# Kernel tuning notes

Hardware: AMD Instinct MI355X
Metric: run time of the kernel (lower is better)

The kernel has to match this reference:

```python
import jax, jax.numpy as jnp
import numpy as np

EPS = 1e-5


def _bn_silu(x, gamma, beta):
    # train-mode BatchNorm2d (biased batch stats over N,H,W) followed by SiLU
    m = jnp.mean(x, axis=(0, 2, 3), keepdims=True)
    v = jnp.var(x, axis=(0, 2, 3), keepdims=True)
    y = gamma[None, :, None, None] * (x - m) * jax.lax.rsqrt(v + EPS) + beta[None, :, None, None]
    return y * jax.nn.sigmoid(y)


def _deform_conv2d(x, offset, w, b):
    # x: [B,C,H,W]; offset: [B,2*9,H,W] as (dy,dx) pairs per 3x3 tap; w: [Co,C,3,3]
    B, C, H, W = x.shape
    Co = w.shape[0]
    off = offset.reshape(B, 9, 2, H, W)
    k = jnp.arange(9)
    ky = (k // 3 - 1).astype(x.dtype)  # kernel tap offsets, pad=1 so centered
    kx = (k % 3 - 1).astype(x.dtype)
    py = jnp.arange(H, dtype=x.dtype)[None, None, :, None] + ky[None, :, None, None] + off[:, :, 0]
    px = jnp.arange(W, dtype=x.dtype)[None, None, None, :] + kx[None, :, None, None] + off[:, :, 1]
    y0 = jnp.floor(py)
    x0 = jnp.floor(px)
    wy1 = py - y0
    wx1 = px - x0
    xf = x.reshape(B, C, H * W)

    def corner(yi, xi, cw):
        # zero-padded bilinear corner: mask out-of-bounds taps via weight
        valid = (yi >= 0) & (yi < H) & (xi >= 0) & (xi < W)
        idx = jnp.clip(yi, 0, H - 1) * W + jnp.clip(xi, 0, W - 1)
        g = jnp.take_along_axis(xf, idx.reshape(B, 1, -1), axis=2).reshape(B, C, 9, H, W)
        return g * (cw * valid.astype(x.dtype))[:, None]

    y0i = y0.astype(jnp.int32)
    x0i = x0.astype(jnp.int32)
    s = corner(y0i, x0i, (1 - wy1) * (1 - wx1))
    s = s + corner(y0i, x0i + 1, (1 - wy1) * wx1)
    s = s + corner(y0i + 1, x0i, wy1 * (1 - wx1))
    s = s + corner(y0i + 1, x0i + 1, wy1 * wx1)
    out = jnp.einsum('bckhw,ock->bohw', s, w.reshape(Co, C, 9))
    return out + b[None, :, None, None]


def _conv_transpose(x, w, stride, pad):
    # torch ConvTranspose2d: weight layout [Cin, Cout, kh, kw]
    k = w.shape[2]
    wf = jnp.flip(w, (2, 3)).transpose(1, 0, 2, 3)  # -> OIHW, spatially flipped
    p = k - 1 - pad
    return jax.lax.conv_general_dilated(
        x, wf, (1, 1), [(p, p), (p, p)], lhs_dilation=(stride, stride),
        dimension_numbers=('NCHW', 'OIHW', 'NCHW'))


def setup_inputs() -> dict:
    key = jax.random.key(0)
    ks = jax.random.split(key, 4)
    B, C, Co, H, W = 16, 256, 256, 32, 32
    r = lambda k, s, sc: jax.random.normal(k, s, jnp.float32) * sc
    return {
        'x': r(ks[0], (B, C, H, W), 1.0),
        'w_off': r(ks[1], (18, C, 3, 3), 0.01),
        'b_off': jnp.zeros((18,), jnp.float32),
        'w_def': r(ks[2], (Co, C, 3, 3), 0.02),
        'b_def': jnp.zeros((Co,), jnp.float32),
        'gamma1': jnp.ones((Co,), jnp.float32),
        'beta1': jnp.zeros((Co,), jnp.float32),
        'w_dc': r(ks[3], (Co, Co, 4, 4), 0.02),
        'gamma2': jnp.ones((Co,), jnp.float32),
        'beta2': jnp.zeros((Co,), jnp.float32),
    }


def reference(x, w_off, b_off, w_def, b_def, gamma1, beta1, w_dc, gamma2, beta2):
    offset = jax.lax.conv_general_dilated(
        x, w_off, (1, 1), [(1, 1), (1, 1)],
        dimension_numbers=('NCHW', 'OIHW', 'NCHW')) + b_off[None, :, None, None]
    y = _deform_conv2d(x, offset, w_def, b_def)
    y = _bn_silu(y, gamma1, beta1)
    y = _conv_transpose(y, w_dc, 2, 1)
    return _bn_silu(y, gamma2, beta2)
```

## Files before the change

### kernel.cpp

```cpp
#include <hip/hip_runtime.h>
#include <math.h>

#ifdef __has_builtin
#if __has_builtin(__builtin_amdgcn_global_load_lds)
#define HAS_GLL 1
#endif
#endif
#ifndef HAS_GLL
#define HAS_GLL 0
#endif

typedef __attribute__((ext_vector_type(8))) short short8v;
typedef __attribute__((ext_vector_type(4))) float float4v;

__device__ __forceinline__ unsigned short f2bf(float f) {
    unsigned int u = __float_as_uint(f);
    u += 0x7fffu + ((u >> 16) & 1u);
    return (unsigned short)(u >> 16);
}

__device__ __forceinline__ float silu(float y) { return y / (1.f + expf(-y)); }

__device__ __forceinline__ void stage1k(const void* gsrc, void* ldsbase) {
#if HAS_GLL
    __builtin_amdgcn_global_load_lds((const __attribute__((address_space(1))) unsigned int*)gsrc,
                                     (__attribute__((address_space(3))) unsigned int*)ldsbase,
                                     16, 0, 0);
#else
    int lane = threadIdx.x & 63;
    *(float4*)((char*)ldsbase + lane * 16) = *(const float4*)gsrc;
#endif
}

__global__ __launch_bounds__(256) void k_prep_all(const float* __restrict__ w_def,
                                                  const float* __restrict__ w_dc,
                                                  const float* __restrict__ w_off,
                                                  const float* __restrict__ x,
                                                  unsigned short* __restrict__ A1,
                                                  unsigned short* __restrict__ A2,
                                                  unsigned short* __restrict__ A2off,
                                                  unsigned short* __restrict__ xT) {
    int blk = blockIdx.x;
    int t = threadIdx.x;
    __shared__ unsigned short tl[32][36];
    if (blk < 4096) {
        int i = blk * 256 + t;
        int ci = i & 255;
        int tq = (i >> 8) & 3;
        int co = (i >> 10) & 255;
        int p  = i >> 18;
        int ph = p >> 1, pw = p & 1;
        int ty = tq >> 1, tx = tq & 1;
        int kh = 2 * ty + 1 - ph;
        int kw = 2 * tx + 1 - pw;
        A2[i] = f2bf(w_dc[((ci * 256 + co) * 4 + kh) * 4 + kw]);
    } else if (blk < 6400) {
        int i = (blk - 4096) * 256 + t;
        A1[i] = f2bf(w_def[i]);
    } else if (blk < 6688) {
        int i = (blk - 6400) * 256 + t;
        int slot = i & 31;
        int oc = (i >> 5) & 31;
        int rest = i >> 10;
        int tap = rest % 9;
        int cc8 = rest / 9;
        int cgrp = (slot >> 3) ^ ((oc >> 1) & 3);
        int c = cc8 * 32 + (cgrp << 3) + (slot & 7);
        unsigned short v = 0;
        if (oc < 18) v = f2bf(w_off[(size_t)oc * 2304 + c * 9 + tap]);
        A2off[i] = v;
    } else {
        int blk2 = blk - 6688;
        int hw0 = (blk2 & 31) * 32;
        int c0 = ((blk2 >> 5) & 7) * 32;
        int b = blk2 >> 8;
        {
            int c_l = t >> 3, w4 = (t & 7) * 4;
            float4 v = *(const float4*)&x[(size_t)((b * 256 + c0 + c_l) * 1024) + hw0 + w4];
            tl[c_l][w4 + 0] = f2bf(v.x);
            tl[c_l][w4 + 1] = f2bf(v.y);
            tl[c_l][w4 + 2] = f2bf(v.z);
            tl[c_l][w4 + 3] = f2bf(v.w);
        }
        __syncthreads();
        {
            int hw_l = t >> 3, c4 = (t & 7) * 4;
            unsigned int s0 = tl[c4 + 0][hw_l];
            unsigned int s1 = tl[c4 + 1][hw_l];
            unsigned int s2 = tl[c4 + 2][hw_l];
            unsigned int s3 = tl[c4 + 3][hw_l];
            uint2 pk;
            pk.x = s0 | (s1 << 16);
            pk.y = s2 | (s3 << 16);
            *(uint2*)&xT[(size_t)((b * 1024 + hw0 + hw_l) * 256) + c0 + c4] = pk;
        }
    }
}

__global__ __launch_bounds__(256) void k_off_gemm(const unsigned short* __restrict__ A2off,
                                                  const unsigned short* __restrict__ xT,
                                                  const float* __restrict__ b_off,
                                                  float* __restrict__ off) {
    int hp = blockIdx.x, b = blockIdx.y;
    int h0 = hp * 2;
    int t = threadIdx.x;
    int lane = t & 63, wid = t >> 6;
    int l15 = lane & 15, g = lane >> 4;
    int swg = (l15 >> 1) & 3;
    __shared__ __align__(16) unsigned short As[9 * 32 * 32];
    __shared__ __align__(16) unsigned short Bsx[4 * 34 * 32];
    float4v acc[2];
    float4v z = {0.f, 0.f, 0.f, 0.f};
    acc[0] = z; acc[1] = z;

    int pos = wid * 16 + l15;
    int py = pos >> 5, px = pos & 31;

    for (int cc8 = 0; cc8 < 8; ++cc8) {
        __syncthreads();
        for (int idx = t; idx < 1152; idx += 256)
            stage1k(A2off + (size_t)cc8 * 9216 + idx * 8, (char*)As + idx * 16);
        for (int idx = t; idx < 544; idx += 256) {
            int r = idx / 136;
            int rem = idx - r * 136;
            int col = rem >> 2;
            int sgrp = rem & 3;
            int grp = sgrp ^ ((col >> 1) & 3);
            int h = h0 - 1 + r;
            int w = col - 1;
            uint4 v = {0u, 0u, 0u, 0u};
            if (h >= 0 && h < 32 && w >= 0 && w < 32)
                v = *(const uint4*)&xT[(size_t)((b * 1024 + h * 32 + w) * 256) + cc8 * 32 + grp * 8];
            *(uint4*)((char*)Bsx + ((r * 34 + col) << 6) + (sgrp << 4)) = v;
        }
        __syncthreads();
#pragma unroll
        for (int tap = 0; tap < 9; ++tap) {
            int ky = tap / 3, kx = tap - ky * 3;
            int col = px + kx;
            int rowr = py + ky;
            short8v bbf = *(const short8v*)((const char*)Bsx + ((rowr * 34 + col) << 6) +
                                            ((g ^ ((col >> 1) & 3)) << 4));
            short8v a0 = *(const short8v*)((const char*)As + tap * 2048 + l15 * 64 + ((g ^ swg) << 4));
            short8v a1 = *(const short8v*)((const char*)As + tap * 2048 + (16 + l15) * 64 + ((g ^ swg) << 4));
            acc[0] = __builtin_amdgcn_mfma_f32_16x16x32_bf16(a0, bbf, acc[0], 0, 0, 0);
            acc[1] = __builtin_amdgcn_mfma_f32_16x16x32_bf16(a1, bbf, acc[1], 0, 0, 0);
        }
    }
    int h = h0 + py;
#pragma unroll
    for (int r = 0; r < 4; ++r) {
        int oc = g * 4 + r;
        off[((size_t)(b * 18 + oc) << 10) + (h << 5) + px] = acc[0][r] + b_off[oc];
    }
    if (g == 0) {
#pragma unroll
        for (int r = 0; r < 2; ++r) {
            int oc = 16 + r;
            off[((size_t)(b * 18 + oc) << 10) + (h << 5) + px] = acc[1][r] + b_off[oc];
        }
    }
}

__global__ __launch_bounds__(576) void k_sample(const float* __restrict__ x,
                                                const float* __restrict__ off,
                                                unsigned short* __restrict__ S) {
    int cg = blockIdx.x, b = blockIdx.y, half = blockIdx.z;
    int cbase = cg * 8;
    int t = threadIdx.x;
    int k = t >> 6, lane = t & 63;
    __shared__ __align__(16) unsigned int xpl[4 * 1156];
    __shared__ __align__(16) unsigned short sS[72 * 66];

    for (int u = t; u < 1024; u += 576) {
        int p = u >> 8, row = (u >> 3) & 31, cq = (u & 7) << 2;
        const float* src0 = x + ((size_t)(b * 256 + cbase + 2 * p) << 10) + (row << 5) + cq;
        float4 a = *(const float4*)src0;
        float4 c = *(const float4*)(src0 + 1024);
        uint4 pk;
        pk.x = (unsigned int)f2bf(a.x) | ((unsigned int)f2bf(c.x) << 16);
        pk.y = (unsigned int)f2bf(a.y) | ((unsigned int)f2bf(c.y) << 16);
        pk.z = (unsigned int)f2bf(a.z) | ((unsigned int)f2bf(c.z) << 16);
        pk.w = (unsigned int)f2bf(a.w) | ((unsigned int)f2bf(c.w) << 16);
        *(uint4*)&xpl[p * 1156 + row * 36 + cq] = pk;
    }

    int wr_row = t / 9, wr_q = t - wr_row * 9;
    const float* offk0 = off + ((size_t)(b * 18 + 2 * k) << 10);
    const float* offk1 = off + ((size_t)(b * 18 + 2 * k + 1) << 10);
    int ky = k / 3 - 1, kx = k % 3 - 1;
    __syncthreads();

    for (int ci = 0; ci < 8; ++ci) {
        int chunk = half * 8 + ci;
        int pos = chunk * 64 + lane;
        int h = pos >> 5, w = pos & 31;
        float dy = offk0[pos];
        float dx = offk1[pos];
        float py = (float)(h + ky) + dy;
        float px = (float)(w + kx) + dx;
        float fy = floorf(py), fx = floorf(px);
        int y0i = (int)fy, x0i = (int)fx;
        float wy = py - fy, wxf = px - fx;
        float vy0 = (y0i >= 0 && y0i < 32) ? 1.f : 0.f;
        float vy1 = (y0i >= -1 && y0i < 31) ? 1.f : 0.f;
        float vx0 = (x0i >= 0 && x0i < 32) ? 1.f : 0.f;
        float vx1 = (x0i >= -1 && x0i < 31) ? 1.f : 0.f;
        int y0c = min(max(y0i, 0), 31), y1c = min(max(y0i + 1, 0), 31);
        int x0c = min(max(x0i, 0), 31), x1c = min(max(x0i + 1, 0), 31);
        float w00 = (1.f - wy) * (1.f - wxf) * vy0 * vx0;
        float w01 = (1.f - wy) * wxf * vy0 * vx1;
        float w10 = wy * (1.f - wxf) * vy1 * vx0;
        float w11 = wy * wxf * vy1 * vx1;
        int a00 = y0c * 36 + x0c, a01 = y0c * 36 + x1c;
        int a10 = y1c * 36 + x0c, a11 = y1c * 36 + x1c;
#pragma unroll
        for (int p = 0; p < 4; ++p) {
            const unsigned int* pl = xpl + p * 1156;
            unsigned int c00 = pl[a00], c01 = pl[a01], c10 = pl[a10], c11 = pl[a11];
            float e00 = __uint_as_float(c00 << 16), o00 = __uint_as_float(c00 & 0xFFFF0000u);
            float e01 = __uint_as_float(c01 << 16), o01 = __uint_as_float(c01 & 0xFFFF0000u);
            float e10 = __uint_as_float(c10 << 16), o10 = __uint_as_float(c10 & 0xFFFF0000u);
            float e11 = __uint_as_float(c11 << 16), o11 = __uint_as_float(c11 & 0xFFFF0000u);
            float ve = w00 * e00 + w01 * e01 + w10 * e10 + w11 * e11;
            float vo = w00 * o00 + w01 * o01 + w10 * o10 + w11 * o11;
            sS[((2 * p) * 9 + k) * 66 + lane] = f2bf(ve);
            sS[((2 * p + 1) * 9 + k) * 66 + lane] = f2bf(vo);
        }
        __syncthreads();
        {
            int basekc = wr_q * 8;
            unsigned int s0 = sS[(basekc + 0) * 66 + wr_row];
            unsigned int s1 = sS[(basekc + 1) * 66 + wr_row];
            unsigned int s2 = sS[(basekc + 2) * 66 + wr_row];
            unsigned int s3 = sS[(basekc + 3) * 66 + wr_row];
            unsigned int s4 = sS[(basekc + 4) * 66 + wr_row];
            unsigned int s5 = sS[(basekc + 5) * 66 + wr_row];
            unsigned int s6 = sS[(basekc + 6) * 66 + wr_row];
            unsigned int s7 = sS[(basekc + 7) * 66 + wr_row];
            uint4 qv;
            qv.x = s0 | (s1 << 16);
            qv.y = s2 | (s3 << 16);
            qv.z = s4 | (s5 << 16);
            qv.w = s6 | (s7 << 16);
            *(uint4*)(S + (size_t)(b * 1024 + chunk * 64 + wr_row) * 2304 + cg * 72 + wr_q * 8) = qv;
        }
        __syncthreads();
    }
}

__global__ __launch_bounds__(256) void k_gemm1(const unsigned short* __restrict__ A1,
                                               const unsigned short* __restrict__ S,
                                               const float* __restrict__ b_def,
                                               float* __restrict__ y1,
                                               float* __restrict__ pstats1) {
    int nb = blockIdx.x, mb = blockIdx.y;
    int t = threadIdx.x;
    int lane = t & 63, wid = t >> 6;
    int wm = wid >> 1, wn = wid & 1;
    int l15 = lane & 15, g = lane >> 4;
    __shared__ __align__(16) unsigned short As[2][8192];
    __shared__ __align__(16) unsigned short Bs[2][4096];
    int m0 = mb * 128, n0 = nb * 64;
    int b = n0 >> 10, pos0 = n0 & 1023;

    const unsigned short* srcA[4];
    int dA[4];
    const unsigned short* srcB[2];
    int dB[2];
#pragma unroll
    for (int it = 0; it < 4; ++it) {
        int idx = t + it * 256;
        int r = idx >> 3, s8 = idx & 7, c = s8 ^ (r & 7);
        srcA[it] = A1 + (size_t)(m0 + r) * 2304 + c * 8;
        dA[it] = idx * 8;
    }
#pragma unroll
    for (int it = 0; it < 2; ++it) {
        int idx = t + it * 256;
        int r = idx >> 3, s8 = idx & 7, c = s8 ^ (r & 7);
        srcB[it] = S + (size_t)(n0 + r) * 2304 + c * 8;
        dB[it] = idx * 8;
    }

    float4v acc[4][2];
    float4v z = {0.f, 0.f, 0.f, 0.f};
#pragma unroll
    for (int i = 0; i < 4; ++i) { acc[i][0] = z; acc[i][1] = z; }

#pragma unroll
    for (int it = 0; it < 4; ++it) stage1k(srcA[it], &As[0][dA[it]]);
#pragma unroll
    for (int it = 0; it < 2; ++it) stage1k(srcB[it], &Bs[0][dB[it]]);
    __syncthreads();

    for (int step = 0; step < 36; ++step) {
        int cur = step & 1;
        if (step < 35) {
            int koff = (step + 1) * 64;
#pragma unroll
            for (int it = 0; it < 4; ++it) stage1k(srcA[it] + koff, &As[cur ^ 1][dA[it]]);
#pragma unroll
            for (int it = 0; it < 2; ++it) stage1k(srcB[it] + koff, &Bs[cur ^ 1][dB[it]]);
        }
        __builtin_amdgcn_s_setprio(1);
#pragma unroll
        for (int kk = 0; kk < 2; ++kk) {
            short8v a[4], bb[2];
#pragma unroll
            for (int mi = 0; mi < 4; ++mi) {
                int row = wm * 64 + mi * 16 + l15;
                int slot = ((kk << 2) + g) ^ (row & 7);
                a[mi] = *(const short8v*)((const char*)&As[cur][0] + row * 128 + slot * 16);
            }
#pragma unroll
            for (int ni = 0; ni < 2; ++ni) {
                int row = wn * 32 + ni * 16 + l15;
                int slot = ((kk << 2) + g) ^ (row & 7);
                bb[ni] = *(const short8v*)((const char*)&Bs[cur][0] + row * 128 + slot * 16);
            }
#pragma unroll
            for (int mi = 0; mi < 4; ++mi)
#pragma unroll
                for (int ni = 0; ni < 2; ++ni)
                    acc[mi][ni] = __builtin_amdgcn_mfma_f32_16x16x32_bf16(a[mi], bb[ni], acc[mi][ni], 0, 0, 0);
        }
        __builtin_amdgcn_s_setprio(0);
        __syncthreads();
    }

    float* sred  = (float*)&As[0][0];
    float* s2red = sred + 256;
#pragma unroll
    for (int mi = 0; mi < 4; ++mi) {
#pragma unroll
        for (int r = 0; r < 4; ++r) {
            int co = m0 + wm * 64 + mi * 16 + g * 4 + r;
            float bv = b_def[co];
            float* dst = y1 + ((size_t)(b * 256 + co) << 10) + pos0;
            float s = 0.f, s2 = 0.f;
#pragma unroll
            for (int ni = 0; ni < 2; ++ni) {
                float v = acc[mi][ni][r] + bv;
                dst[wn * 32 + ni * 16 + l15] = v;
                s += v;
                s2 += v * v;
            }
#pragma unroll
            for (int m = 8; m >= 1; m >>= 1) {
                s  += __shfl_xor(s, m, 64);
                s2 += __shfl_xor(s2, m, 64);
            }
            if (l15 == 0) {
                int col = wm * 64 + mi * 16 + g * 4 + r;
                sred[col * 2 + wn]  = s;
                s2red[col * 2 + wn] = s2;
            }
        }
    }
    __syncthreads();
    if (t < 128) {
        float s  = sred[t * 2] + sred[t * 2 + 1];
        float s2 = s2red[t * 2] + s2red[t * 2 + 1];
        int ch = m0 + t;
        pstats1[ch * 256 + nb] = s;
        pstats1[65536 + ch * 256 + nb] = s2;
    }
}

__global__ __launch_bounds__(256) void k_gemm2(const unsigned short* __restrict__ A2,
                                               const unsigned short* __restrict__ y1T,
                                               unsigned short* __restrict__ outP,
                                               float* __restrict__ pstats2) {
    int nb = blockIdx.x, mb = blockIdx.y, p = blockIdx.z;
    int ph = p >> 1, pw = p & 1;
    int t = threadIdx.x;
    int lane = t & 63, wid = t >> 6;
    int wm = wid >> 1, wn = wid & 1;
    int l15 = lane & 15, g = lane >> 4;
    __shared__ __align__(16) unsigned short As[2][8192];
    __shared__ __align__(16) unsigned short Bs[2][8192];
    int m0 = mb * 128, n0 = nb * 128;
    int b = n0 >> 10, pos0 = n0 & 1023, oh0 = pos0 >> 5;

    int dtab[4];
#pragma unroll
    for (int tap = 0; tap < 4; ++tap) {
        int ty = tap >> 1, tx = tap & 1;
        int dy = ph ? (1 - ty) : (-ty);
        int dx = pw ? (1 - tx) : (-tx);
        dtab[tap] = (dy * 34 + dx) * 256;
    }
    const unsigned short* srcA[4];
    const unsigned short* srcB[4];
    int dstoff[4];
#pragma unroll
    for (int it = 0; it < 4; ++it) {
        int idx = t + it * 256;
        int r = idx >> 3, s8 = idx & 7, c = s8 ^ (r & 7);
        srcA[it] = A2 + (size_t)(p * 256 + m0 + r) * 1024 + c * 8;
        int ih = oh0 + (r >> 5) + 1;
        int iw = (r & 31) + 1;
        srcB[it] = y1T + ((size_t)(b * 34 + ih) * 34 + iw) * 256 + c * 8;
        dstoff[it] = idx * 8;
    }

    float4v acc[4][4];
    float4v z = {0.f, 0.f, 0.f, 0.f};
#pragma unroll
    for (int i = 0; i < 4; ++i)
#pragma unroll
        for (int j = 0; j < 4; ++j) acc[i][j] = z;

#pragma unroll
    for (int it = 0; it < 4; ++it) {
        stage1k(srcA[it], &As[0][dstoff[it]]);
        stage1k(srcB[it] + dtab[0], &Bs[0][dstoff[it]]);
    }
    __syncthreads();

#pragma unroll
    for (int step = 0; step < 16; ++step) {
        int cur = step & 1;
        if (step < 15) {
            int ns = step + 1;
            int tap = ns >> 2;
            int koff = ns * 64;
            int boff = dtab[tap] + (ns & 3) * 64;
#pragma unroll
            for (int it = 0; it < 4; ++it) {
                stage1k(srcA[it] + koff, &As[cur ^ 1][dstoff[it]]);
                stage1k(srcB[it] + boff, &Bs[cur ^ 1][dstoff[it]]);
            }
        }
        __builtin_amdgcn_s_setprio(1);
#pragma unroll
        for (int kk = 0; kk < 2; ++kk) {
            short8v a[4], bb[4];
#pragma unroll
            for (int mi = 0; mi < 4; ++mi) {
                int row = wm * 64 + mi * 16 + l15;
                int slot = ((kk << 2) + g) ^ (row & 7);
                a[mi] = *(const short8v*)((const char*)&As[cur][0] + row * 128 + slot * 16);
            }
#pragma unroll
            for (int ni = 0; ni < 4; ++ni) {
                int row = wn * 64 + ni * 16 + l15;
                int slot = ((kk << 2) + g) ^ (row & 7);
                bb[ni] = *(const short8v*)((const char*)&Bs[cur][0] + row * 128 + slot * 16);
            }
#pragma unroll
            for (int mi = 0; mi < 4; ++mi)
#pragma unroll
                for (int ni = 0; ni < 4; ++ni)
                    acc[mi][ni] = __builtin_amdgcn_mfma_f32_16x16x32_bf16(a[mi], bb[ni], acc[mi][ni], 0, 0, 0);
        }
        __builtin_amdgcn_s_setprio(0);
        __syncthreads();
    }
#pragma unroll
    for (int mi = 0; mi < 4; ++mi) {
#pragma unroll
        for (int r = 0; r < 4; ++r) {
            int co = m0 + wm * 64 + mi * 16 + g * 4 + r;
            unsigned short* dst = outP + ((size_t)((p * 16 + b) * 256 + co) << 10) + pos0;
#pragma unroll
            for (int ni = 0; ni < 4; ++ni)
                dst[wn * 64 + ni * 16 + l15] = f2bf(acc[mi][ni][r]);
        }
    }
    float* sred  = (float*)&As[0][0];
    float* s2red = sred + 256;
#pragma unroll
    for (int mi = 0; mi < 4; ++mi) {
#pragma unroll
        for (int r = 0; r < 4; ++r) {
            float s = 0.f, s2 = 0.f;
#pragma unroll
            for (int ni = 0; ni < 4; ++ni) {
                float v = acc[mi][ni][r];
                s += v;
                s2 += v * v;
            }
#pragma unroll
            for (int m = 8; m >= 1; m >>= 1) {
                s  += __shfl_xor(s, m, 64);
                s2 += __shfl_xor(s2, m, 64);
            }
            if (l15 == 0) {
                int col = wm * 64 + mi * 16 + g * 4 + r;
                sred[col * 2 + wn]  = s;
                s2red[col * 2 + wn] = s2;
            }
        }
    }
    __syncthreads();
    if (t < 128) {
        float s  = sred[t * 2] + sred[t * 2 + 1];
        float s2 = s2red[t * 2] + s2red[t * 2 + 1];
        int row = p * 128 + nb;
        int ch = m0 + t;
        pstats2[ch * 512 + row] = s;
        pstats2[131072 + ch * 512 + row] = s2;
    }
}

__global__ __launch_bounds__(256) void k_bnfin_par(const float* __restrict__ pstats, int nparts,
                                                   float n,
                                                   float* __restrict__ mean, float* __restrict__ rstd) {
    int ch = blockIdx.x;
    int t = threadIdx.x;
    float s = 0.f, s2 = 0.f;
    for (int j = t; j < nparts; j += 256) {
        s  += pstats[ch * nparts + j];
        s2 += pstats[256 * nparts + ch * nparts + j];
    }
    __shared__ float rs[256], rs2[256];
    rs[t] = s; rs2[t] = s2;
    __syncthreads();
    for (int d = 128; d > 0; d >>= 1) {
        if (t < d) { rs[t] += rs[t + d]; rs2[t] += rs2[t + d]; }
        __syncthreads();
    }
    if (t == 0) {
        float m = rs[0] / n;
        float var = rs2[0] / n - m * m;
        mean[ch] = m;
        rstd[ch] = rsqrtf(var + 1e-5f);
    }
}

__global__ __launch_bounds__(256) void k_bnsilu_padT(const float* __restrict__ y1,
                                                     const float* __restrict__ mean,
                                                     const float* __restrict__ rstd,
                                                     const float* __restrict__ gamma,
                                                     const float* __restrict__ beta,
                                                     unsigned short* __restrict__ y1T) {
    int py = blockIdx.x, cg = blockIdx.y, b = blockIdx.z;
    int c0 = cg * 32;
    int t = threadIdx.x;
    uint2 zz; zz.x = 0u; zz.y = 0u;
    if (py == 0 || py == 33) {
        for (int u = t; u < 272; u += 256) {
            int col = u >> 3, c4 = (u & 7) * 4;
            *(uint2*)&y1T[((size_t)(b * 34 + py) * 34 + col) * 256 + c0 + c4] = zz;
        }
        return;
    }
    __shared__ unsigned short tl[32][36];
    int iy = py - 1;
    {
        int c_l = t >> 3, px4 = (t & 7) * 4;
        int ch = c0 + c_l;
        float m = mean[ch], rs = rstd[ch], ga = gamma[ch], be = beta[ch];
        float4 v = *(const float4*)&y1[(size_t)((b * 256 + ch) << 10) + (iy << 5) + px4];
        tl[c_l][px4 + 0] = f2bf(silu(ga * (v.x - m) * rs + be));
        tl[c_l][px4 + 1] = f2bf(silu(ga * (v.y - m) * rs + be));
        tl[c_l][px4 + 2] = f2bf(silu(ga * (v.z - m) * rs + be));
        tl[c_l][px4 + 3] = f2bf(silu(ga * (v.w - m) * rs + be));
    }
    __syncthreads();
    {
        int px = t >> 3, c4 = (t & 7) * 4;
        unsigned int s0 = tl[c4 + 0][px];
        unsigned int s1 = tl[c4 + 1][px];
        unsigned int s2 = tl[c4 + 2][px];
        unsigned int s3 = tl[c4 + 3][px];
        uint2 pk;
        pk.x = s0 | (s1 << 16);
        pk.y = s2 | (s3 << 16);
        *(uint2*)&y1T[((size_t)(b * 34 + py) * 34 + (px + 1)) * 256 + c0 + c4] = pk;
    }
    if (t < 16) {
        int col = (t >> 3) ? 33 : 0;
        int c4 = (t & 7) * 4;
        *(uint2*)&y1T[((size_t)(b * 34 + py) * 34 + col) * 256 + c0 + c4] = zz;
    }
}

__global__ __launch_bounds__(256) void k_bnsilu_out(const unsigned short* __restrict__ outP,
                                                    const float* __restrict__ mean,
                                                    const float* __restrict__ rstd,
                                                    const float* __restrict__ gamma,
                                                    const float* __restrict__ beta,
                                                    float* __restrict__ out) {
    unsigned int i = blockIdx.x * 256 + threadIdx.x;
    int ow4 = i & 15;
    int oh = (i >> 4) & 63;
    int co = (i >> 10) & 255;
    int b  = i >> 18;
    int p0 = (oh & 1) * 2;
    int pos = ((oh >> 1) << 5) + ow4 * 2;
    const unsigned short* pl0 = outP + ((size_t)((p0 * 16 + b) * 256 + co) << 10) + pos;
    const unsigned short* pl1 = pl0 + ((size_t)16 * 256 << 10);
    unsigned int ue = *(const unsigned int*)pl0;
    unsigned int uo = *(const unsigned int*)pl1;
    float ex = __uint_as_float(ue << 16), ey = __uint_as_float(ue & 0xFFFF0000u);
    float ox = __uint_as_float(uo << 16), oy = __uint_as_float(uo & 0xFFFF0000u);
    float m = mean[co], rs = rstd[co], ga = gamma[co], be = beta[co];
    float4 v;
    v.x = silu(ga * (ex - m) * rs + be);
    v.y = silu(ga * (ox - m) * rs + be);
    v.z = silu(ga * (ey - m) * rs + be);
    v.w = silu(ga * (oy - m) * rs + be);
    *(float4*)&out[((size_t)(b * 256 + co) << 12) + (oh << 6) + ow4 * 4] = v;
}

extern "C" void kernel_launch(void* const* d_in, const int* in_sizes, int n_in,
                              void* d_out, int out_size, void* d_ws, size_t ws_size,
                              hipStream_t stream) {
    const float* x      = (const float*)d_in[0];
    const float* w_off  = (const float*)d_in[1];
    const float* b_off  = (const float*)d_in[2];
    const float* w_def  = (const float*)d_in[3];
    const float* b_def  = (const float*)d_in[4];
    const float* gamma1 = (const float*)d_in[5];
    const float* beta1  = (const float*)d_in[6];
    const float* w_dc   = (const float*)d_in[7];
    const float* gamma2 = (const float*)d_in[8];
    const float* beta2  = (const float*)d_in[9];
    float* out = (float*)d_out;

    char* base = (char*)d_ws;
    unsigned short* S    = (unsigned short*)base;
    float*          y1   = (float*)(base + 75497472);
    unsigned short* y1T  = (unsigned short*)(base + 92274688);
    unsigned short* A1   = (unsigned short*)(base + 101744640);
    unsigned short* A2   = (unsigned short*)(base + 102924288);
    float*          off  = (float*)(base + 105021440);
    float*          stats = (float*)(base + 106201088);
    float* mean1 = stats, *rstd1 = stats + 256, *mean2 = stats + 512, *rstd2 = stats + 768;
    float* pstats1 = off;
    float* pstats2 = off;
    unsigned short* xT    = (unsigned short*)base;
    unsigned short* A2off = (unsigned short*)(base + 8388608);
    unsigned short* outP = (unsigned short*)base;

    k_prep_all<<<10784, 256, 0, stream>>>(w_def, w_dc, w_off, x, A1, A2, A2off, xT);
    k_off_gemm<<<dim3(16, 16), 256, 0, stream>>>(A2off, xT, b_off, off);
    k_sample<<<dim3(32, 16, 2), 576, 0, stream>>>(x, off, S);
    k_gemm1<<<dim3(256, 2), 256, 0, stream>>>(A1, S, b_def, y1, pstats1);
    k_bnfin_par<<<256, 256, 0, stream>>>(pstats1, 256, 16384.f, mean1, rstd1);
    k_bnsilu_padT<<<dim3(34, 8, 16), 256, 0, stream>>>(y1, mean1, rstd1, gamma1, beta1, y1T);
    k_gemm2<<<dim3(128, 2, 4), 256, 0, stream>>>(A2, y1T, outP, pstats2);
    k_bnfin_par<<<256, 256, 0, stream>>>(pstats2, 512, 65536.f, mean2, rstd2);
    k_bnsilu_out<<<16384, 256, 0, stream>>>(outP, mean2, rstd2, gamma2, beta2, out);
}
```

Measured before the change: 185.4 us.

## Switch GEMMs to 32x32x16 MFMA and store pre-BN activation as bf16

Both GEMM kernels move from 16x16x32 to 32x32x16 bf16 MFMA tiles. This cuts the number of LDS fragment loads per MFMA and reworks the epilogue indexing and the shuffle reductions to match the 32-lane layout. Separately, the deform-conv output y1 is written as bf16 instead of fp32, halving the intermediate traffic between gemm1 and the BN/SiLU kernel. The risk is slightly lower precision in the pre-BN values, while the BN statistics are still computed in fp32.

```diff
diff --git a/kernel.cpp b/kernel.cpp
--- a/kernel.cpp
+++ b/kernel.cpp
@@ -12,6 +12,7 @@
 
 typedef __attribute__((ext_vector_type(8))) short short8v;
 typedef __attribute__((ext_vector_type(4))) float float4v;
+typedef __attribute__((ext_vector_type(16))) float float16v;
 
 __device__ __forceinline__ unsigned short f2bf(float f) {
     unsigned int u = __float_as_uint(f);
@@ -252,13 +253,13 @@
 __global__ __launch_bounds__(256) void k_gemm1(const unsigned short* __restrict__ A1,
                                                const unsigned short* __restrict__ S,
                                                const float* __restrict__ b_def,
-                                               float* __restrict__ y1,
+                                               unsigned short* __restrict__ y1b,
                                                float* __restrict__ pstats1) {
     int nb = blockIdx.x, mb = blockIdx.y;
     int t = threadIdx.x;
     int lane = t & 63, wid = t >> 6;
     int wm = wid >> 1, wn = wid & 1;
-    int l15 = lane & 15, g = lane >> 4;
+    int l31 = lane & 31, hh = lane >> 5;
     __shared__ __align__(16) unsigned short As[2][8192];
     __shared__ __align__(16) unsigned short Bs[2][4096];
     int m0 = mb * 128, n0 = nb * 64;
@@ -283,10 +284,11 @@
         dB[it] = idx * 8;
     }
 
-    float4v acc[4][2];
-    float4v z = {0.f, 0.f, 0.f, 0.f};
-#pragma unroll
-    for (int i = 0; i < 4; ++i) { acc[i][0] = z; acc[i][1] = z; }
+    float16v acc[2];
+#pragma unroll
+    for (int i = 0; i < 2; ++i)
+#pragma unroll
+        for (int j = 0; j < 16; ++j) acc[i][j] = 0.f;
 
 #pragma unroll
     for (int it = 0; it < 4; ++it) stage1k(srcA[it], &As[0][dA[it]]);
@@ -305,25 +307,17 @@
         }
         __builtin_amdgcn_s_setprio(1);
 #pragma unroll
-        for (int kk = 0; kk < 2; ++kk) {
-            short8v a[4], bb[2];
-#pragma unroll
-            for (int mi = 0; mi < 4; ++mi) {
-                int row = wm * 64 + mi * 16 + l15;
-                int slot = ((kk << 2) + g) ^ (row & 7);
-                a[mi] = *(const short8v*)((const char*)&As[cur][0] + row * 128 + slot * 16);
-            }
-#pragma unroll
-            for (int ni = 0; ni < 2; ++ni) {
-                int row = wn * 32 + ni * 16 + l15;
-                int slot = ((kk << 2) + g) ^ (row & 7);
-                bb[ni] = *(const short8v*)((const char*)&Bs[cur][0] + row * 128 + slot * 16);
-            }
-#pragma unroll
-            for (int mi = 0; mi < 4; ++mi)
-#pragma unroll
-                for (int ni = 0; ni < 2; ++ni)
-                    acc[mi][ni] = __builtin_amdgcn_mfma_f32_16x16x32_bf16(a[mi], bb[ni], acc[mi][ni], 0, 0, 0);
+        for (int kk = 0; kk < 4; ++kk) {
+            int browR = wn * 32 + l31;
+            int bslot = ((kk << 1) + hh) ^ (browR & 7);
+            short8v bb = *(const short8v*)((const char*)&Bs[cur][0] + browR * 128 + bslot * 16);
+#pragma unroll
+            for (int mi = 0; mi < 2; ++mi) {
+                int row = wm * 64 + mi * 32 + l31;
+                int slot = ((kk << 1) + hh) ^ (row & 7);
+                short8v a = *(const short8v*)((const char*)&As[cur][0] + row * 128 + slot * 16);
+                acc[mi] = __builtin_amdgcn_mfma_f32_32x32x16_bf16(a, bb, acc[mi], 0, 0, 0);
+            }
         }
         __builtin_amdgcn_s_setprio(0);
         __syncthreads();
@@ -332,27 +326,21 @@
     float* sred  = (float*)&As[0][0];
     float* s2red = sred + 256;
 #pragma unroll
-    for (int mi = 0; mi < 4; ++mi) {
-#pragma unroll
-        for (int r = 0; r < 4; ++r) {
-            int co = m0 + wm * 64 + mi * 16 + g * 4 + r;
-            float bv = b_def[co];
-            float* dst = y1 + ((size_t)(b * 256 + co) << 10) + pos0;
-            float s = 0.f, s2 = 0.f;
-#pragma unroll
-            for (int ni = 0; ni < 2; ++ni) {
-                float v = acc[mi][ni][r] + bv;
-                dst[wn * 32 + ni * 16 + l15] = v;
-                s += v;
-                s2 += v * v;
-            }
-#pragma unroll
-            for (int m = 8; m >= 1; m >>= 1) {
+    for (int mi = 0; mi < 2; ++mi) {
+#pragma unroll
+        for (int reg = 0; reg < 16; ++reg) {
+            int rowf = (reg & 3) + 8 * (reg >> 2) + 4 * hh;
+            int co = m0 + wm * 64 + mi * 32 + rowf;
+            float v = acc[mi][reg] + b_def[co];
+            y1b[((size_t)(b * 256 + co) << 10) + pos0 + wn * 32 + l31] = f2bf(v);
+            float s = v, s2 = v * v;
+#pragma unroll
+            for (int m = 16; m >= 1; m >>= 1) {
                 s  += __shfl_xor(s, m, 64);
                 s2 += __shfl_xor(s2, m, 64);
             }
-            if (l15 == 0) {
-                int col = wm * 64 + mi * 16 + g * 4 + r;
+            if (l31 == 0) {
+                int col = co - m0;
                 sred[col * 2 + wn]  = s;
                 s2red[col * 2 + wn] = s2;
             }
@@ -377,7 +365,7 @@
     int t = threadIdx.x;
     int lane = t & 63, wid = t >> 6;
     int wm = wid >> 1, wn = wid & 1;
-    int l15 = lane & 15, g = lane >> 4;
+    int l31 = lane & 31, hh = lane >> 5;
     __shared__ __align__(16) unsigned short As[2][8192];
     __shared__ __align__(16) unsigned short Bs[2][8192];
     int m0 = mb * 128, n0 = nb * 128;
@@ -405,12 +393,13 @@
         dstoff[it] = idx * 8;
     }
 
-    float4v acc[4][4];
-    float4v z = {0.f, 0.f, 0.f, 0.f};
-#pragma unroll
-    for (int i = 0; i < 4; ++i)
-#pragma unroll
-        for (int j = 0; j < 4; ++j) acc[i][j] = z;
+    float16v acc[2][2];
+#pragma unroll
+    for (int i = 0; i < 2; ++i)
+#pragma unroll
+        for (int j = 0; j < 2; ++j)
+#pragma unroll
+            for (int q = 0; q < 16; ++q) acc[i][j][q] = 0.f;
 
 #pragma unroll
     for (int it = 0; it < 4; ++it) {
@@ -435,60 +424,59 @@
         }
         __builtin_amdgcn_s_setprio(1);
 #pragma unroll
-        for (int kk = 0; kk < 2; ++kk) {
-            short8v a[4], bb[4];
-#pragma unroll
-            for (int mi = 0; mi < 4; ++mi) {
-                int row = wm * 64 + mi * 16 + l15;
-                int slot = ((kk << 2) + g) ^ (row & 7);
+        for (int kk = 0; kk < 4; ++kk) {
+            short8v a[2], bb[2];
+#pragma unroll
+            for (int mi = 0; mi < 2; ++mi) {
+                int row = wm * 64 + mi * 32 + l31;
+                int slot = ((kk << 1) + hh) ^ (row & 7);
                 a[mi] = *(const short8v*)((const char*)&As[cur][0] + row * 128 + slot * 16);
             }
 #pragma unroll
-            for (int ni = 0; ni < 4; ++ni) {
-                int row = wn * 64 + ni * 16 + l15;
-                int slot = ((kk << 2) + g) ^ (row & 7);
+            for (int ni = 0; ni < 2; ++ni) {
+                int row = wn * 64 + ni * 32 + l31;
+                int slot = ((kk << 1) + hh) ^ (row & 7);
                 bb[ni] = *(const short8v*)((const char*)&Bs[cur][0] + row * 128 + slot * 16);
             }
 #pragma unroll
-            for (int mi = 0; mi < 4; ++mi)
-#pragma unroll
-                for (int ni = 0; ni < 4; ++ni)
-                    acc[mi][ni] = __builtin_amdgcn_mfma_f32_16x16x32_bf16(a[mi], bb[ni], acc[mi][ni], 0, 0, 0);
+            for (int mi = 0; mi < 2; ++mi)
+#pragma unroll
+                for (int ni = 0; ni < 2; ++ni)
+                    acc[mi][ni] = __builtin_amdgcn_mfma_f32_32x32x16_bf16(a[mi], bb[ni], acc[mi][ni], 0, 0, 0);
         }
         __builtin_amdgcn_s_setprio(0);
         __syncthreads();
     }
 #pragma unroll
-    for (int mi = 0; mi < 4; ++mi) {
-#pragma unroll
-        for (int r = 0; r < 4; ++r) {
-            int co = m0 + wm * 64 + mi * 16 + g * 4 + r;
+    for (int mi = 0; mi < 2; ++mi) {
+#pragma unroll
+        for (int reg = 0; reg < 16; ++reg) {
+            int rowf = (reg & 3) + 8 * (reg >> 2) + 4 * hh;
+            int co = m0 + wm * 64 + mi * 32 + rowf;
             unsigned short* dst = outP + ((size_t)((p * 16 + b) * 256 + co) << 10) + pos0;
 #pragma unroll
-            for (int ni = 0; ni < 4; ++ni)
-                dst[wn * 64 + ni * 16 + l15] = f2bf(acc[mi][ni][r]);
+            for (int ni = 0; ni < 2; ++ni)
+                dst[wn * 64 + ni * 32 + l31] = f2bf(acc[mi][ni][reg]);
         }
     }
     float* sred  = (float*)&As[0][0];
     float* s2red = sred + 256;
 #pragma unroll
-    for (int mi = 0; mi < 4; ++mi) {
-#pragma unroll
-        for (int r = 0; r < 4; ++r) {
-            float s = 0.f, s2 = 0.f;
-#pragma unroll
-            for (int ni = 0; ni < 4; ++ni) {
-                float v = acc[mi][ni][r];
-                s += v;
-                s2 += v * v;
-            }
-#pragma unroll
-            for (int m = 8; m >= 1; m >>= 1) {
+    for (int mi = 0; mi < 2; ++mi) {
+#pragma unroll
+        for (int reg = 0; reg < 16; ++reg) {
+            int rowf = (reg & 3) + 8 * (reg >> 2) + 4 * hh;
+            float v0 = acc[mi][0][reg];
+            float v1 = acc[mi][1][reg];
+            float s = v0 + v1;
+            float s2 = v0 * v0 + v1 * v1;
+#pragma unroll
+            for (int m = 16; m >= 1; m >>= 1) {
                 s  += __shfl_xor(s, m, 64);
                 s2 += __shfl_xor(s2, m, 64);
             }
-            if (l15 == 0) {
-                int col = wm * 64 + mi * 16 + g * 4 + r;
+            if (l31 == 0) {
+                int col = wm * 64 + mi * 32 + rowf;
                 sred[col * 2 + wn]  = s;
                 s2red[col * 2 + wn] = s2;
             }
@@ -530,7 +518,7 @@
     }
 }
 
-__global__ __launch_bounds__(256) void k_bnsilu_padT(const float* __restrict__ y1,
+__global__ __launch_bounds__(256) void k_bnsilu_padT(const unsigned short* __restrict__ y1b,
                                                      const float* __restrict__ mean,
                                                      const float* __restrict__ rstd,
                                                      const float* __restrict__ gamma,
@@ -553,11 +541,13 @@
         int c_l = t >> 3, px4 = (t & 7) * 4;
         int ch = c0 + c_l;
         float m = mean[ch], rs = rstd[ch], ga = gamma[ch], be = beta[ch];
-        float4 v = *(const float4*)&y1[(size_t)((b * 256 + ch) << 10) + (iy << 5) + px4];
-        tl[c_l][px4 + 0] = f2bf(silu(ga * (v.x - m) * rs + be));
-        tl[c_l][px4 + 1] = f2bf(silu(ga * (v.y - m) * rs + be));
-        tl[c_l][px4 + 2] = f2bf(silu(ga * (v.z - m) * rs + be));
-        tl[c_l][px4 + 3] = f2bf(silu(ga * (v.w - m) * rs + be));
+        uint2 v = *(const uint2*)&y1b[(size_t)((b * 256 + ch) << 10) + (iy << 5) + px4];
+        float f0 = __uint_as_float(v.x << 16), f1 = __uint_as_float(v.x & 0xFFFF0000u);
+        float f2 = __uint_as_float(v.y << 16), f3 = __uint_as_float(v.y & 0xFFFF0000u);
+        tl[c_l][px4 + 0] = f2bf(silu(ga * (f0 - m) * rs + be));
+        tl[c_l][px4 + 1] = f2bf(silu(ga * (f1 - m) * rs + be));
+        tl[c_l][px4 + 2] = f2bf(silu(ga * (f2 - m) * rs + be));
+        tl[c_l][px4 + 3] = f2bf(silu(ga * (f3 - m) * rs + be));
     }
     __syncthreads();
     {
@@ -623,7 +613,7 @@
 
     char* base = (char*)d_ws;
     unsigned short* S    = (unsigned short*)base;
-    float*          y1   = (float*)(base + 75497472);
+    unsigned short* y1b  = (unsigned short*)(base + 75497472);
     unsigned short* y1T  = (unsigned short*)(base + 92274688);
     unsigned short* A1   = (unsigned short*)(base + 101744640);
     unsigned short* A2   = (unsigned short*)(base + 102924288);
@@ -639,9 +629,9 @@
     k_prep_all<<<10784, 256, 0, stream>>>(w_def, w_dc, w_off, x, A1, A2, A2off, xT);
     k_off_gemm<<<dim3(16, 16), 256, 0, stream>>>(A2off, xT, b_off, off);
     k_sample<<<dim3(32, 16, 2), 576, 0, stream>>>(x, off, S);
-    k_gemm1<<<dim3(256, 2), 256, 0, stream>>>(A1, S, b_def, y1, pstats1);
+    k_gemm1<<<dim3(256, 2), 256, 0, stream>>>(A1, S, b_def, y1b, pstats1);
     k_bnfin_par<<<256, 256, 0, stream>>>(pstats1, 256, 16384.f, mean1, rstd1);
-    k_bnsilu_padT<<<dim3(34, 8, 16), 256, 0, stream>>>(y1, mean1, rstd1, gamma1, beta1, y1T);
+    k_bnsilu_padT<<<dim3(34, 8, 16), 256, 0, stream>>>(y1b, mean1, rstd1, gamma1, beta1, y1T);
     k_gemm2<<<dim3(128, 2, 4), 256, 0, stream>>>(A2, y1T, outP, pstats2);
     k_bnfin_par<<<256, 256, 0, stream>>>(pstats2, 512, 65536.f, mean2, rstd2);
     k_bnsilu_out<<<16384, 256, 0, stream>>>(outP, mean2, rstd2, gamma2, beta2, out);
```

Result: slower. 198.9 us (+7.3%).
